# Performance work log

Measured on AMD Instinct MI355X. Metric: run time of the kernel, lower is better.

Reference implementation:

```python
import jax, jax.numpy as jnp
import numpy as np

N, H, W = 8, 512, 512
C = 16
TEX = 1024
LEVELS = 4
SH_START = 3


def setup_inputs() -> dict:
    key = jax.random.key(0)
    ks = jax.random.split(key, 2 + LEVELS)
    d = {
        "uv_map": jax.random.uniform(ks[0], (N, H, W, 2), dtype=jnp.float32),
        "sh_basis_map": jax.random.normal(ks[1], (N, H, W, 9), dtype=jnp.float32),
    }
    for i in range(LEVELS):
        s = int(round(TEX / 2.0 ** i))
        d[f"tex{i}"] = jax.random.normal(ks[2 + i], (s, s, C), dtype=jnp.float32) * 0.05
    return d


def _grid_sample_bilinear(tex, uv):
    """torch.grid_sample(mode=bilinear, padding=zeros, align_corners=False),
    grid built as (2u-1, -(2v-1)). tex: [Ht,Wt,C]; uv: [N,H,W,2] in [0,1].
    Returns [N,H,W,C]."""
    Ht, Wt, _ = tex.shape
    gx = uv[..., 0] * 2.0 - 1.0
    gy = -(uv[..., 1] * 2.0 - 1.0)  # y flip from original code
    ix = ((gx + 1.0) * Wt - 1.0) * 0.5  # unnormalize, align_corners=False
    iy = ((gy + 1.0) * Ht - 1.0) * 0.5
    ix0 = jnp.floor(ix); iy0 = jnp.floor(iy)
    ix1 = ix0 + 1.0;     iy1 = iy0 + 1.0
    wx1 = ix - ix0; wx0 = 1.0 - wx1
    wy1 = iy - iy0; wy0 = 1.0 - wy1

    def gather(iyf, ixf):
        iyi = iyf.astype(jnp.int32)
        ixi = ixf.astype(jnp.int32)
        valid = ((iyi >= 0) & (iyi < Ht) & (ixi >= 0) & (ixi < Wt))
        v = tex[jnp.clip(iyi, 0, Ht - 1), jnp.clip(ixi, 0, Wt - 1)]  # [N,H,W,C]
        return v * valid[..., None].astype(tex.dtype)  # zeros padding

    out = (gather(iy0, ix0) * (wy0 * wx0)[..., None]
           + gather(iy0, ix1) * (wy0 * wx1)[..., None]
           + gather(iy1, ix0) * (wy1 * wx0)[..., None]
           + gather(iy1, ix1) * (wy1 * wx1)[..., None])
    return out


def reference(uv_map, sh_basis_map, tex0, tex1, tex2, tex3):
    # accumulate all mipmap levels sampled at the same uv grid
    out = _grid_sample_bilinear(tex0, uv_map)
    for tex in (tex1, tex2, tex3):
        out = out + _grid_sample_bilinear(tex, uv_map)
    # mask pixels where u == 0
    mask = (uv_map[..., 0] == 0.0)[..., None]
    out = jnp.where(mask, 0.0, out)
    # SH multiply on channels [SH_START : SH_START+9]
    out = jnp.concatenate(
        [out[..., :SH_START],
         out[..., SH_START:SH_START + 9] * sh_basis_map,
         out[..., SH_START + 9:]], axis=-1)
    return out.transpose(0, 3, 1, 2)  # [N, C, H, W]
```

## Files before the change

### kernel.cpp

```cpp
#include <hip/hip_runtime.h>

#define NB 8
#define H 512
#define W 512
#define HW (H * W)
#define C 16
#define NPIX (NB * HW)
#define SH_START 3

#define G 32
#define NBINS (G * G)
#define CAP 3072
#define DUMPSLOT (NBINS * CAP)

#define BS_BLOCKS 256
#define BS_THREADS 1024
#define PXB (NPIX / BS_BLOCKS)
#define KPT (PXB / BS_THREADS)

#define OFF_INTER  ((size_t)0)
#define OFF_UV     ((size_t)100663360)
#define OFF_SLOT   ((size_t)125829248)
#define OFF_CUR    ((size_t)134217856)
#define WS_NEED    ((size_t)134221952)

#define D0 0
#define D1 (1156 * 8)
#define D2 ((1156 + 324) * 8)
#define D3 ((1156 + 324 + 100) * 8)
#define LDS_DWORDS ((1156 + 324 + 100 + 36) * 8)

typedef float f32x4 __attribute__((ext_vector_type(4)));
typedef unsigned int u32x2 __attribute__((ext_vector_type(2)));

__device__ __forceinline__ int bin_of(float u, float v) {
    int bx = (int)(u * (float)G);
    int by = (int)(v * (float)G);
    bx = bx < 0 ? 0 : (bx > G - 1 ? G - 1 : bx);
    by = by < 0 ? 0 : (by > G - 1 ? G - 1 : by);
    return by * G + bx;
}

__device__ __forceinline__ unsigned int f2bf(float f) {
    unsigned int u = __float_as_uint(f);
    unsigned int r = (u + 0x7FFFu + ((u >> 16) & 1u)) >> 16;
    return r & 0xFFFFu;
}

__global__ __launch_bounds__(BS_THREADS) void binsort_kernel(const float* __restrict__ uv,
                                                             int* __restrict__ cur,
                                                             float2* __restrict__ uvr,
                                                             int* __restrict__ slotmap) {
    __shared__ f32x4 stage[PXB];
    __shared__ int h[NBINS];
    __shared__ int lstart[NBINS];
    __shared__ int gbase[NBINS];
    __shared__ int wsum[16];
    int tid = threadIdx.x;
    int wv = tid >> 6;
    int lane = tid & 63;
    int pbase = blockIdx.x * PXB;
    const float2* uv2 = reinterpret_cast<const float2*>(uv);

    float2 p[KPT];
    int bn[KPT];
    h[tid] = 0;
    __syncthreads();
#pragma unroll
    for (int k = 0; k < KPT; ++k) {
        p[k] = uv2[pbase + tid + k * BS_THREADS];
        bn[k] = bin_of(p[k].x, p[k].y);
        atomicAdd(&h[bn[k]], 1);
    }
    __syncthreads();
    int cnt = h[tid];
    gbase[tid] = atomicAdd(&cur[tid], cnt);
    int x = cnt;
#pragma unroll
    for (int off = 1; off < 64; off <<= 1) {
        int up = __shfl_up(x, off);
        if (lane >= off) x += up;
    }
    if (lane == 63) wsum[wv] = x;
    __syncthreads();
    if (wv == 0 && lane < 16) {
        int y = wsum[lane];
#pragma unroll
        for (int off = 1; off < 16; off <<= 1) {
            int up = __shfl_up(y, off);
            if (lane >= off) y += up;
        }
        wsum[lane] = y;
    }
    __syncthreads();
    int wbase = (wv > 0) ? wsum[wv - 1] : 0;
    lstart[tid] = wbase + x - cnt;
    h[tid] = 0;
    __syncthreads();
#pragma unroll
    for (int k = 0; k < KPT; ++k) {
        int b = bn[k];
        int r = atomicAdd(&h[b], 1);
        int ls = lstart[b] + r;
        int within = gbase[b] + r;
        int gs = (within < CAP) ? (b * CAP + within) : DUMPSLOT;
        slotmap[pbase + tid + k * BS_THREADS] = gs;
        f32x4 rec;
        rec.x = p[k].x;
        rec.y = p[k].y;
        rec.z = 0.0f;
        rec.w = __int_as_float(gs);
        stage[ls] = rec;
    }
    __syncthreads();
#pragma unroll
    for (int k = 0; k < KPT; ++k) {
        f32x4 rec = stage[tid + k * BS_THREADS];
        int gs = __float_as_int(rec.w);
        uvr[gs] = make_float2(rec.x, rec.y);
    }
}

template<int S, int N>
__device__ __forceinline__ void stage_mip_bf16(const float* __restrict__ t,
                                               unsigned int* __restrict__ lbase,
                                               int x0, int y0, int tid) {
    for (int i = tid; i < N * N * 4; i += 512) {
        int tx = i >> 2, ch = i & 3;
        int ly = tx / N, lx = tx - ly * N;
        int gy = y0 + ly, gx = x0 + lx;
        u32x2 d = {0u, 0u};
        if (gy >= 0 && gy < S && gx >= 0 && gx < S) {
            f32x4 val = *reinterpret_cast<const f32x4*>(t + ((size_t)(gy * S + gx)) * C + ch * 4);
            d.x = f2bf(val.x) | (f2bf(val.y) << 16);
            d.y = f2bf(val.z) | (f2bf(val.w) << 16);
        }
        *reinterpret_cast<u32x2*>(lbase + (ly * N + lx) * 8 + ch * 2) = d;
    }
}

#define BFL(x) __uint_as_float((x) << 16)
#define BFH(x) __uint_as_float((x) & 0xFFFF0000u)

template<int S, int N>
__device__ __forceinline__ void sample_mip_bf16(const unsigned int* __restrict__ lbase,
                                                int x0, int y0,
                                                float u, float v, int ch2, f32x4& acc) {
    float Sf = (float)S;
    float gx = u * 2.0f - 1.0f;
    float gy = -(v * 2.0f - 1.0f);
    float ix = ((gx + 1.0f) * Sf - 1.0f) * 0.5f;
    float iy = ((gy + 1.0f) * Sf - 1.0f) * 0.5f;
    float ix0f = floorf(ix);
    float iy0f = floorf(iy);
    float wx1 = ix - ix0f;
    float wy1 = iy - iy0f;
    float wx0 = 1.0f - wx1;
    float wy0 = 1.0f - wy1;
    int lx = (int)ix0f - x0;
    int ly = (int)iy0f - y0;
    const unsigned int* p = lbase + (ly * N + lx) * 8 + ch2;
    u32x2 d00 = *reinterpret_cast<const u32x2*>(p);
    u32x2 d01 = *reinterpret_cast<const u32x2*>(p + 8);
    u32x2 d10 = *reinterpret_cast<const u32x2*>(p + 8 * N);
    u32x2 d11 = *reinterpret_cast<const u32x2*>(p + 8 * N + 8);
    float w00 = wy0 * wx0, w01 = wy0 * wx1, w10 = wy1 * wx0, w11 = wy1 * wx1;
    acc.x = fmaf(BFL(d00.x), w00, acc.x);
    acc.y = fmaf(BFH(d00.x), w00, acc.y);
    acc.z = fmaf(BFL(d00.y), w00, acc.z);
    acc.w = fmaf(BFH(d00.y), w00, acc.w);
    acc.x = fmaf(BFL(d01.x), w01, acc.x);
    acc.y = fmaf(BFH(d01.x), w01, acc.y);
    acc.z = fmaf(BFL(d01.y), w01, acc.z);
    acc.w = fmaf(BFH(d01.y), w01, acc.w);
    acc.x = fmaf(BFL(d10.x), w10, acc.x);
    acc.y = fmaf(BFH(d10.x), w10, acc.y);
    acc.z = fmaf(BFL(d10.y), w10, acc.z);
    acc.w = fmaf(BFH(d10.y), w10, acc.w);
    acc.x = fmaf(BFL(d11.x), w11, acc.x);
    acc.y = fmaf(BFH(d11.x), w11, acc.y);
    acc.z = fmaf(BFL(d11.y), w11, acc.z);
    acc.w = fmaf(BFH(d11.y), w11, acc.w);
}

__global__ __launch_bounds__(512) void phaseA_kernel(
    const float2* __restrict__ uvr, const int* __restrict__ cur,
    const float* __restrict__ t0, const float* __restrict__ t1,
    const float* __restrict__ t2, const float* __restrict__ t3,
    unsigned int* __restrict__ inter) {
    __shared__ unsigned int lds[LDS_DWORDS];
    int blk = blockIdx.x;
    int bin = (blk & 7) * (NBINS / 8) + (blk >> 3);
    int bx = bin & (G - 1), by = bin >> 5;
    int tid = threadIdx.x;

    int cnt = cur[bin];
    if (cnt > CAP) cnt = CAP;
    int start = bin * CAP;

    const int x0_0 = bx * 32 - 1, y0_0 = 1024 - (by + 1) * 32 - 1;
    const int x0_1 = bx * 16 - 1, y0_1 = 512  - (by + 1) * 16 - 1;
    const int x0_2 = bx * 8  - 1, y0_2 = 256  - (by + 1) * 8  - 1;
    const int x0_3 = bx * 4  - 1, y0_3 = 128  - (by + 1) * 4  - 1;

    stage_mip_bf16<1024, 34>(t0, lds + D0, x0_0, y0_0, tid);
    stage_mip_bf16<512,  18>(t1, lds + D1, x0_1, y0_1, tid);
    stage_mip_bf16<256,  10>(t2, lds + D2, x0_2, y0_2, tid);
    stage_mip_bf16<128,   6>(t3, lds + D3, x0_3, y0_3, tid);
    __syncthreads();

    int wave = tid >> 6;
    int lane = tid & 63;
    int q    = lane >> 2;
    int chq  = lane & 3;
    int ch2  = chq * 2;

    if (cnt <= 0) return;

    int i0 = wave * 16;
    int cm1 = cnt - 1;
    int i = i0 + q;
    float2 ruv = uvr[start + (i < cm1 ? i : cm1)];
    while (i0 < cnt) {
        int ni0 = i0 + 8 * 16;
        float2 nuv = ruv;
        if (ni0 < cnt) {
            int ni = ni0 + q;
            nuv = uvr[start + (ni < cm1 ? ni : cm1)];
        }
        float u = ruv.x, v = ruv.y;

        f32x4 a0 = {0.0f, 0.0f, 0.0f, 0.0f};
        f32x4 a1 = {0.0f, 0.0f, 0.0f, 0.0f};
        f32x4 a2 = {0.0f, 0.0f, 0.0f, 0.0f};
        f32x4 a3 = {0.0f, 0.0f, 0.0f, 0.0f};
        sample_mip_bf16<1024, 34>(lds + D0, x0_0, y0_0, u, v, ch2, a0);
        sample_mip_bf16<512,  18>(lds + D1, x0_1, y0_1, u, v, ch2, a1);
        sample_mip_bf16<256,  10>(lds + D2, x0_2, y0_2, u, v, ch2, a2);
        sample_mip_bf16<128,   6>(lds + D3, x0_3, y0_3, u, v, ch2, a3);
        f32x4 acc = (a0 + a1) + (a2 + a3);

        if (u == 0.0f) acc = (f32x4){0.0f, 0.0f, 0.0f, 0.0f};

        if (i0 + q < cnt) {
            u32x2 pk;
            pk.x = f2bf(acc.x) | (f2bf(acc.y) << 16);
            pk.y = f2bf(acc.z) | (f2bf(acc.w) << 16);
            u32x2* op = reinterpret_cast<u32x2*>(inter) + (size_t)(start + i0 + q) * 4 + chq;
            *op = pk;
        }
        ruv = nuv;
        i0 = ni0;
    }
}

__global__ __launch_bounds__(256) void phaseB_kernel(const unsigned int* __restrict__ inter,
                                                     const int* __restrict__ slotmap,
                                                     const float* __restrict__ sh,
                                                     float* __restrict__ out) {
    __shared__ float shs[256 * 9];
    int base = blockIdx.x * 256;
    const float* shp = sh + (size_t)base * 9;
    for (int i = threadIdx.x; i < 256 * 9; i += 256) shs[i] = shp[i];
    __syncthreads();

    int pix = base + threadIdx.x;
    int slot = slotmap[pix];
    const uint4* ip = reinterpret_cast<const uint4*>(inter) + (size_t)slot * 2;
    uint4 a = ip[0];
    uint4 b = ip[1];
    float c0  = BFL(a.x), c1  = BFH(a.x), c2  = BFL(a.y), c3  = BFH(a.y);
    float c4  = BFL(a.z), c5  = BFH(a.z), c6  = BFL(a.w), c7  = BFH(a.w);
    float c8  = BFL(b.x), c9  = BFH(b.x), c10 = BFL(b.y), c11 = BFH(b.y);
    float c12 = BFL(b.z), c13 = BFH(b.z), c14 = BFL(b.w), c15 = BFH(b.w);
    const float* s = &shs[threadIdx.x * 9];
    c3  *= s[0];
    c4  *= s[1]; c5  *= s[2]; c6  *= s[3]; c7  *= s[4];
    c8  *= s[5]; c9  *= s[6]; c10 *= s[7]; c11 *= s[8];

    int n  = pix >> 18;
    int hw = pix & (HW - 1);
    float* op = out + (size_t)n * C * HW + hw;
    __builtin_nontemporal_store(c0,  op + 0 * HW);
    __builtin_nontemporal_store(c1,  op + 1 * HW);
    __builtin_nontemporal_store(c2,  op + 2 * HW);
    __builtin_nontemporal_store(c3,  op + 3 * HW);
    __builtin_nontemporal_store(c4,  op + 4 * HW);
    __builtin_nontemporal_store(c5,  op + 5 * HW);
    __builtin_nontemporal_store(c6,  op + 6 * HW);
    __builtin_nontemporal_store(c7,  op + 7 * HW);
    __builtin_nontemporal_store(c8,  op + (size_t)8 * HW);
    __builtin_nontemporal_store(c9,  op + (size_t)9 * HW);
    __builtin_nontemporal_store(c10, op + (size_t)10 * HW);
    __builtin_nontemporal_store(c11, op + (size_t)11 * HW);
    __builtin_nontemporal_store(c12, op + (size_t)12 * HW);
    __builtin_nontemporal_store(c13, op + (size_t)13 * HW);
    __builtin_nontemporal_store(c14, op + (size_t)14 * HW);
    __builtin_nontemporal_store(c15, op + (size_t)15 * HW);
}

__device__ __forceinline__ void tap(const float* __restrict__ t, int S, int iy, int ix,
                                    float w, float acc[C]) {
    if (iy >= 0 && iy < S && ix >= 0 && ix < S) {
        const float4* p = reinterpret_cast<const float4*>(t + ((size_t)iy * S + ix) * C);
        float4 q0 = p[0];
        float4 q1 = p[1];
        float4 q2 = p[2];
        float4 q3 = p[3];
        acc[0]  = fmaf(q0.x, w, acc[0]);
        acc[1]  = fmaf(q0.y, w, acc[1]);
        acc[2]  = fmaf(q0.z, w, acc[2]);
        acc[3]  = fmaf(q0.w, w, acc[3]);
        acc[4]  = fmaf(q1.x, w, acc[4]);
        acc[5]  = fmaf(q1.y, w, acc[5]);
        acc[6]  = fmaf(q1.z, w, acc[6]);
        acc[7]  = fmaf(q1.w, w, acc[7]);
        acc[8]  = fmaf(q2.x, w, acc[8]);
        acc[9]  = fmaf(q2.y, w, acc[9]);
        acc[10] = fmaf(q2.z, w, acc[10]);
        acc[11] = fmaf(q2.w, w, acc[11]);
        acc[12] = fmaf(q3.x, w, acc[12]);
        acc[13] = fmaf(q3.y, w, acc[13]);
        acc[14] = fmaf(q3.z, w, acc[14]);
        acc[15] = fmaf(q3.w, w, acc[15]);
    }
}

__device__ __forceinline__ void sample_level(const float* __restrict__ t, int S,
                                             float u, float v, float acc[C]) {
    float Sf = (float)S;
    float gx = u * 2.0f - 1.0f;
    float gy = -(v * 2.0f - 1.0f);
    float ix = ((gx + 1.0f) * Sf - 1.0f) * 0.5f;
    float iy = ((gy + 1.0f) * Sf - 1.0f) * 0.5f;
    float ix0f = floorf(ix);
    float iy0f = floorf(iy);
    float wx1 = ix - ix0f;
    float wy1 = iy - iy0f;
    float wx0 = 1.0f - wx1;
    float wy0 = 1.0f - wy1;
    int ix0 = (int)ix0f;
    int iy0 = (int)iy0f;
    tap(t, S, iy0,     ix0,     wy0 * wx0, acc);
    tap(t, S, iy0,     ix0 + 1, wy0 * wx1, acc);
    tap(t, S, iy0 + 1, ix0,     wy1 * wx0, acc);
    tap(t, S, iy0 + 1, ix0 + 1, wy1 * wx1, acc);
}

__global__ __launch_bounds__(256) void texmap_kernel(
    const float* __restrict__ uv, const float* __restrict__ sh,
    const float* __restrict__ t0, const float* __restrict__ t1,
    const float* __restrict__ t2, const float* __restrict__ t3,
    float* __restrict__ out) {
    int idx = blockIdx.x * 256 + threadIdx.x;
    if (idx >= NPIX) return;

    float2 uvv = *reinterpret_cast<const float2*>(uv + (size_t)idx * 2);
    float u = uvv.x;
    float v = uvv.y;

    float acc[C];
#pragma unroll
    for (int c = 0; c < C; ++c) acc[c] = 0.0f;

    sample_level(t0, 1024, u, v, acc);
    sample_level(t1, 512,  u, v, acc);
    sample_level(t2, 256,  u, v, acc);
    sample_level(t3, 128,  u, v, acc);

    if (u == 0.0f) {
#pragma unroll
        for (int c = 0; c < C; ++c) acc[c] = 0.0f;
    }

    const float* shp = sh + (size_t)idx * 9;
#pragma unroll
    for (int j = 0; j < 9; ++j) acc[SH_START + j] *= shp[j];

    int n  = idx >> 18;
    int hw = idx & (HW - 1);
    float* op = out + (size_t)n * C * HW + hw;
#pragma unroll
    for (int c = 0; c < C; ++c) {
        __builtin_nontemporal_store(acc[c], op + (size_t)c * HW);
    }
}

extern "C" void kernel_launch(void* const* d_in, const int* in_sizes, int n_in,
                              void* d_out, int out_size, void* d_ws, size_t ws_size,
                              hipStream_t stream) {
    const float* uv = (const float*)d_in[0];
    const float* sh = (const float*)d_in[1];
    const float* t0 = (const float*)d_in[2];
    const float* t1 = (const float*)d_in[3];
    const float* t2 = (const float*)d_in[4];
    const float* t3 = (const float*)d_in[5];
    float* out = (float*)d_out;

    if (ws_size < WS_NEED) {
        texmap_kernel<<<dim3((NPIX + 255) / 256), dim3(256), 0, stream>>>(
            uv, sh, t0, t1, t2, t3, out);
        return;
    }

    char* ws = (char*)d_ws;
    unsigned int* inter   = (unsigned int*)(ws + OFF_INTER);
    float2*       uvr     = (float2*)(ws + OFF_UV);
    int*          slotmap = (int*)(ws + OFF_SLOT);
    int*          cur     = (int*)(ws + OFF_CUR);

    (void)hipMemsetAsync(cur, 0, NBINS * sizeof(int), stream);
    binsort_kernel<<<dim3(BS_BLOCKS), dim3(BS_THREADS), 0, stream>>>(uv, cur, uvr, slotmap);
    phaseA_kernel<<<dim3(NBINS), dim3(512), 0, stream>>>(
        uvr, cur, t0, t1, t2, t3, inter);
    phaseB_kernel<<<dim3(NPIX / 256), dim3(256), 0, stream>>>(inter, slotmap, sh, out);
}
```

Baseline: 160.5 us.

## Switch staged textures and intermediates from bf16 to fp16, reuse atomic ranks, pad LDS

Replaces the manual bf16 rounding and packing with the hardware packed fp16 conversion (cvt_pkrtz) when staging mip tiles in LDS and when writing the intermediate buffer. Unpacking becomes half-to-float conversions in place of shifts and masks. The bin sort now keeps the rank returned by the first histogram atomic instead of running a second atomic pass. Each mip region in LDS gets 16 dwords of padding, likely to change bank alignment. fp16 gives more mantissa but less range, and pkrtz truncates toward zero instead of rounding to nearest. The new unpacks may also cost more ALU work than the old bf16 shifts.

```diff
diff --git a/kernel.cpp b/kernel.cpp
--- a/kernel.cpp
+++ b/kernel.cpp
@@ -24,14 +24,19 @@
 #define OFF_CUR    ((size_t)134217856)
 #define WS_NEED    ((size_t)134221952)
 
+#define SZ0 (1156 * 8 + 16)
+#define SZ1 (324 * 8 + 16)
+#define SZ2 (100 * 8 + 16)
+#define SZ3 (36 * 8 + 16)
 #define D0 0
-#define D1 (1156 * 8)
-#define D2 ((1156 + 324) * 8)
-#define D3 ((1156 + 324 + 100) * 8)
-#define LDS_DWORDS ((1156 + 324 + 100 + 36) * 8)
+#define D1 (D0 + SZ0)
+#define D2 (D1 + SZ1)
+#define D3 (D2 + SZ2)
+#define LDS_DWORDS (D3 + SZ3)
 
 typedef float f32x4 __attribute__((ext_vector_type(4)));
 typedef unsigned int u32x2 __attribute__((ext_vector_type(2)));
+typedef __fp16 h16x2 __attribute__((ext_vector_type(2)));
 
 __device__ __forceinline__ int bin_of(float u, float v) {
     int bx = (int)(u * (float)G);
@@ -41,10 +46,17 @@
     return by * G + bx;
 }
 
-__device__ __forceinline__ unsigned int f2bf(float f) {
-    unsigned int u = __float_as_uint(f);
-    unsigned int r = (u + 0x7FFFu + ((u >> 16) & 1u)) >> 16;
-    return r & 0xFFFFu;
+__device__ __forceinline__ unsigned int pk16(float a, float b) {
+    h16x2 h = __builtin_amdgcn_cvt_pkrtz(a, b);
+    return __builtin_bit_cast(unsigned int, h);
+}
+__device__ __forceinline__ float lo16(unsigned int x) {
+    h16x2 h = __builtin_bit_cast(h16x2, x);
+    return (float)h.x;
+}
+__device__ __forceinline__ float hi16(unsigned int x) {
+    h16x2 h = __builtin_bit_cast(h16x2, x);
+    return (float)h.y;
 }
 
 __global__ __launch_bounds__(BS_THREADS) void binsort_kernel(const float* __restrict__ uv,
@@ -64,13 +76,14 @@
 
     float2 p[KPT];
     int bn[KPT];
+    int rk[KPT];
     h[tid] = 0;
     __syncthreads();
 #pragma unroll
     for (int k = 0; k < KPT; ++k) {
         p[k] = uv2[pbase + tid + k * BS_THREADS];
         bn[k] = bin_of(p[k].x, p[k].y);
-        atomicAdd(&h[bn[k]], 1);
+        rk[k] = atomicAdd(&h[bn[k]], 1);
     }
     __syncthreads();
     int cnt = h[tid];
@@ -95,12 +108,11 @@
     __syncthreads();
     int wbase = (wv > 0) ? wsum[wv - 1] : 0;
     lstart[tid] = wbase + x - cnt;
-    h[tid] = 0;
     __syncthreads();
 #pragma unroll
     for (int k = 0; k < KPT; ++k) {
         int b = bn[k];
-        int r = atomicAdd(&h[b], 1);
+        int r = rk[k];
         int ls = lstart[b] + r;
         int within = gbase[b] + r;
         int gs = (within < CAP) ? (b * CAP + within) : DUMPSLOT;
@@ -122,9 +134,9 @@
 }
 
 template<int S, int N>
-__device__ __forceinline__ void stage_mip_bf16(const float* __restrict__ t,
-                                               unsigned int* __restrict__ lbase,
-                                               int x0, int y0, int tid) {
+__device__ __forceinline__ void stage_mip_f16(const float* __restrict__ t,
+                                              unsigned int* __restrict__ lbase,
+                                              int x0, int y0, int tid) {
     for (int i = tid; i < N * N * 4; i += 512) {
         int tx = i >> 2, ch = i & 3;
         int ly = tx / N, lx = tx - ly * N;
@@ -132,20 +144,17 @@
         u32x2 d = {0u, 0u};
         if (gy >= 0 && gy < S && gx >= 0 && gx < S) {
             f32x4 val = *reinterpret_cast<const f32x4*>(t + ((size_t)(gy * S + gx)) * C + ch * 4);
-            d.x = f2bf(val.x) | (f2bf(val.y) << 16);
-            d.y = f2bf(val.z) | (f2bf(val.w) << 16);
+            d.x = pk16(val.x, val.y);
+            d.y = pk16(val.z, val.w);
         }
         *reinterpret_cast<u32x2*>(lbase + (ly * N + lx) * 8 + ch * 2) = d;
     }
 }
 
-#define BFL(x) __uint_as_float((x) << 16)
-#define BFH(x) __uint_as_float((x) & 0xFFFF0000u)
-
 template<int S, int N>
-__device__ __forceinline__ void sample_mip_bf16(const unsigned int* __restrict__ lbase,
-                                                int x0, int y0,
-                                                float u, float v, int ch2, f32x4& acc) {
+__device__ __forceinline__ void sample_mip_f16(const unsigned int* __restrict__ lbase,
+                                               int x0, int y0,
+                                               float u, float v, int ch2, f32x4& acc) {
     float Sf = (float)S;
     float gx = u * 2.0f - 1.0f;
     float gy = -(v * 2.0f - 1.0f);
@@ -165,22 +174,22 @@
     u32x2 d10 = *reinterpret_cast<const u32x2*>(p + 8 * N);
     u32x2 d11 = *reinterpret_cast<const u32x2*>(p + 8 * N + 8);
     float w00 = wy0 * wx0, w01 = wy0 * wx1, w10 = wy1 * wx0, w11 = wy1 * wx1;
-    acc.x = fmaf(BFL(d00.x), w00, acc.x);
-    acc.y = fmaf(BFH(d00.x), w00, acc.y);
-    acc.z = fmaf(BFL(d00.y), w00, acc.z);
-    acc.w = fmaf(BFH(d00.y), w00, acc.w);
-    acc.x = fmaf(BFL(d01.x), w01, acc.x);
-    acc.y = fmaf(BFH(d01.x), w01, acc.y);
-    acc.z = fmaf(BFL(d01.y), w01, acc.z);
-    acc.w = fmaf(BFH(d01.y), w01, acc.w);
-    acc.x = fmaf(BFL(d10.x), w10, acc.x);
-    acc.y = fmaf(BFH(d10.x), w10, acc.y);
-    acc.z = fmaf(BFL(d10.y), w10, acc.z);
-    acc.w = fmaf(BFH(d10.y), w10, acc.w);
-    acc.x = fmaf(BFL(d11.x), w11, acc.x);
-    acc.y = fmaf(BFH(d11.x), w11, acc.y);
-    acc.z = fmaf(BFL(d11.y), w11, acc.z);
-    acc.w = fmaf(BFH(d11.y), w11, acc.w);
+    acc.x = fmaf(lo16(d00.x), w00, acc.x);
+    acc.y = fmaf(hi16(d00.x), w00, acc.y);
+    acc.z = fmaf(lo16(d00.y), w00, acc.z);
+    acc.w = fmaf(hi16(d00.y), w00, acc.w);
+    acc.x = fmaf(lo16(d01.x), w01, acc.x);
+    acc.y = fmaf(hi16(d01.x), w01, acc.y);
+    acc.z = fmaf(lo16(d01.y), w01, acc.z);
+    acc.w = fmaf(hi16(d01.y), w01, acc.w);
+    acc.x = fmaf(lo16(d10.x), w10, acc.x);
+    acc.y = fmaf(hi16(d10.x), w10, acc.y);
+    acc.z = fmaf(lo16(d10.y), w10, acc.z);
+    acc.w = fmaf(hi16(d10.y), w10, acc.w);
+    acc.x = fmaf(lo16(d11.x), w11, acc.x);
+    acc.y = fmaf(hi16(d11.x), w11, acc.y);
+    acc.z = fmaf(lo16(d11.y), w11, acc.z);
+    acc.w = fmaf(hi16(d11.y), w11, acc.w);
 }
 
 __global__ __launch_bounds__(512) void phaseA_kernel(
@@ -203,10 +212,10 @@
     const int x0_2 = bx * 8  - 1, y0_2 = 256  - (by + 1) * 8  - 1;
     const int x0_3 = bx * 4  - 1, y0_3 = 128  - (by + 1) * 4  - 1;
 
-    stage_mip_bf16<1024, 34>(t0, lds + D0, x0_0, y0_0, tid);
-    stage_mip_bf16<512,  18>(t1, lds + D1, x0_1, y0_1, tid);
-    stage_mip_bf16<256,  10>(t2, lds + D2, x0_2, y0_2, tid);
-    stage_mip_bf16<128,   6>(t3, lds + D3, x0_3, y0_3, tid);
+    stage_mip_f16<1024, 34>(t0, lds + D0, x0_0, y0_0, tid);
+    stage_mip_f16<512,  18>(t1, lds + D1, x0_1, y0_1, tid);
+    stage_mip_f16<256,  10>(t2, lds + D2, x0_2, y0_2, tid);
+    stage_mip_f16<128,   6>(t3, lds + D3, x0_3, y0_3, tid);
     __syncthreads();
 
     int wave = tid >> 6;
@@ -234,18 +243,18 @@
         f32x4 a1 = {0.0f, 0.0f, 0.0f, 0.0f};
         f32x4 a2 = {0.0f, 0.0f, 0.0f, 0.0f};
         f32x4 a3 = {0.0f, 0.0f, 0.0f, 0.0f};
-        sample_mip_bf16<1024, 34>(lds + D0, x0_0, y0_0, u, v, ch2, a0);
-        sample_mip_bf16<512,  18>(lds + D1, x0_1, y0_1, u, v, ch2, a1);
-        sample_mip_bf16<256,  10>(lds + D2, x0_2, y0_2, u, v, ch2, a2);
-        sample_mip_bf16<128,   6>(lds + D3, x0_3, y0_3, u, v, ch2, a3);
+        sample_mip_f16<1024, 34>(lds + D0, x0_0, y0_0, u, v, ch2, a0);
+        sample_mip_f16<512,  18>(lds + D1, x0_1, y0_1, u, v, ch2, a1);
+        sample_mip_f16<256,  10>(lds + D2, x0_2, y0_2, u, v, ch2, a2);
+        sample_mip_f16<128,   6>(lds + D3, x0_3, y0_3, u, v, ch2, a3);
         f32x4 acc = (a0 + a1) + (a2 + a3);
 
         if (u == 0.0f) acc = (f32x4){0.0f, 0.0f, 0.0f, 0.0f};
 
         if (i0 + q < cnt) {
             u32x2 pk;
-            pk.x = f2bf(acc.x) | (f2bf(acc.y) << 16);
-            pk.y = f2bf(acc.z) | (f2bf(acc.w) << 16);
+            pk.x = pk16(acc.x, acc.y);
+            pk.y = pk16(acc.z, acc.w);
             u32x2* op = reinterpret_cast<u32x2*>(inter) + (size_t)(start + i0 + q) * 4 + chq;
             *op = pk;
         }
@@ -269,10 +278,10 @@
     const uint4* ip = reinterpret_cast<const uint4*>(inter) + (size_t)slot * 2;
     uint4 a = ip[0];
     uint4 b = ip[1];
-    float c0  = BFL(a.x), c1  = BFH(a.x), c2  = BFL(a.y), c3  = BFH(a.y);
-    float c4  = BFL(a.z), c5  = BFH(a.z), c6  = BFL(a.w), c7  = BFH(a.w);
-    float c8  = BFL(b.x), c9  = BFH(b.x), c10 = BFL(b.y), c11 = BFH(b.y);
-    float c12 = BFL(b.z), c13 = BFH(b.z), c14 = BFL(b.w), c15 = BFH(b.w);
+    float c0  = lo16(a.x), c1  = hi16(a.x), c2  = lo16(a.y), c3  = hi16(a.y);
+    float c4  = lo16(a.z), c5  = hi16(a.z), c6  = lo16(a.w), c7  = hi16(a.w);
+    float c8  = lo16(b.x), c9  = hi16(b.x), c10 = lo16(b.y), c11 = hi16(b.y);
+    float c12 = lo16(b.z), c13 = hi16(b.z), c14 = lo16(b.w), c15 = hi16(b.w);
     const float* s = &shs[threadIdx.x * 9];
     c3  *= s[0];
     c4  *= s[1]; c5  *= s[2]; c6  *= s[3]; c7  *= s[4];
```

After: 160.9 us. No clear change (+0.3%).
